# Kernel optimization log

Hardware: AMD Instinct MI355X
Metric: run time of the kernel (lower is better)

Reference implementation:

```python
import jax, jax.numpy as jnp
import numpy as np

H = 1024        # hidden_size
I = 512         # moe_intermediate_size
E = 16          # n_routed_experts
K = 2           # num_experts_per_tok
N_SHARED = 2    # n_shared_experts
IS = I * N_SHARED  # shared expert intermediate
B, S = 2, 2048


def setup_inputs() -> dict:
    key = jax.random.key(0)
    ks = jax.random.split(key, 9)
    sc = 0.02
    return {
        "hidden_states": jax.random.normal(ks[0], (B, S, H), jnp.float32),
        "router_w":     jax.random.normal(ks[1], (E, H), jnp.float32) * sc,
        "expert_gate":  jax.random.normal(ks[2], (E, H, I), jnp.float32) * sc,
        "expert_up":    jax.random.normal(ks[3], (E, H, I), jnp.float32) * sc,
        "expert_down":  jax.random.normal(ks[4], (E, I, H), jnp.float32) * sc,
        "shared_gate":  jax.random.normal(ks[5], (H, IS), jnp.float32) * sc,
        "shared_up":    jax.random.normal(ks[6], (H, IS), jnp.float32) * sc,
        "shared_down":  jax.random.normal(ks[7], (IS, H), jnp.float32) * sc,
    }


def reference(hidden_states, router_w, expert_gate, expert_up, expert_down,
              shared_gate, shared_up, shared_down):
    orig_shape = hidden_states.shape
    x = hidden_states.reshape(-1, H)            # [T, H]
    T = x.shape[0]

    # --- MoEGate: softmax router scores, top-k, normalized weights ---
    scores = jax.nn.softmax(x @ router_w.T, axis=-1)        # [T, E]
    topk_w, topk_idx = jax.lax.top_k(scores, K)             # [T, K]
    topk_w = topk_w / jnp.sum(topk_w, axis=-1, keepdims=True)  # norm_topk_prob

    # Sparse combine weights as dense [T, E] gate matrix (scatter of top-k).
    gates = jnp.zeros((T, E), x.dtype).at[jnp.arange(T)[:, None], topk_idx].add(topk_w)

    # --- Routed experts: gated SiLU MLP per expert, weighted combine ---
    g = jnp.einsum('th,ehi->tei', x, expert_gate)           # [T, E, I]
    u = jnp.einsum('th,ehi->tei', x, expert_up)             # [T, E, I]
    a = jax.nn.silu(g) * u                                  # [T, E, I]
    y = jnp.einsum('tei,eih,te->th', a, expert_down, gates) # [T, H]

    # --- Shared experts ---
    s = (jax.nn.silu(x @ shared_gate) * (x @ shared_up)) @ shared_down  # [T, H]

    return (y + s).reshape(orig_shape)
```

## Files before the change

kernel.cpp:

```cpp
#include <hip/hip_runtime.h>
#include <math.h>

#define H_DIM 1024
#define I_DIM 512
#define E_NUM 16
#define T_TOK 4096
#define IS_DIM 1024
#define CSTR 32

#define P_RT   1024
#define P_WU   (P_RT + 2048)
#define P_SG   (P_WU + 2048)
#define P_SU   (P_SG + 256)
#define P_END  (P_SU + 256)

#define G_GEMM 1152
#define G_TR   2304
#define G_END  (G_GEMM + G_TR)

#define D_GRID 896

typedef unsigned short u16;
typedef __attribute__((ext_vector_type(8))) short short8;
typedef __attribute__((ext_vector_type(4))) float floatx4;

__device__ __forceinline__ float bf2f(u16 u) {
    union { unsigned int u; float f; } c; c.u = ((unsigned int)u) << 16; return c.f;
}
__device__ __forceinline__ u16 f2bf(float f) {
    union { float f; unsigned int u; } c; c.f = f;
    unsigned int r = (c.u + 0x7fffu + ((c.u >> 16) & 1u)) >> 16;
    return (u16)r;
}
__device__ __forceinline__ void gld16(const u16* g, u16* l) {
    __builtin_amdgcn_global_load_lds(
        (const __attribute__((address_space(1))) unsigned int*)g,
        (__attribute__((address_space(3))) unsigned int*)l, 16, 0, 0);
}

__device__ __forceinline__ void tr64(const float* src, u16* dst, int R, int C,
                                     int local, u16* tile)
{
    int tpm = (R >> 6) * (C >> 6);
    int mat = local / tpm;
    int tl_ = local - mat * tpm;
    int tcn = C >> 6;
    int tr = tl_ / tcn, tc = tl_ - tr * tcn;
    src += (size_t)mat * R * C;
    dst += (size_t)mat * R * C;
    int t = threadIdx.x;
    int r0 = t >> 2, c0 = (t & 3) << 4;
    const float* sp = src + (size_t)(tr * 64 + r0) * C + tc * 64 + c0;
    #pragma unroll
    for (int j = 0; j < 16; j += 4) {
        float4 v = *(const float4*)(sp + j);
        tile[r0 * 65 + c0 + j + 0] = f2bf(v.x);
        tile[r0 * 65 + c0 + j + 1] = f2bf(v.y);
        tile[r0 * 65 + c0 + j + 2] = f2bf(v.z);
        tile[r0 * 65 + c0 + j + 3] = f2bf(v.w);
    }
    __syncthreads();
    int cW = t >> 2, rW = (t & 3) << 4;
    u16 tmp[16];
    #pragma unroll
    for (int j = 0; j < 16; ++j) tmp[j] = tile[(rW + j) * 65 + cW];
    u16* dp = dst + (size_t)(tc * 64 + cW) * R + tr * 64 + rW;
    *(uint4*)(dp)     = *(const uint4*)(tmp);
    *(uint4*)(dp + 8) = *(const uint4*)(tmp + 8);
}

__device__ __forceinline__ int derive_routed(int gi, const int* cnt,
                                             int& e, int& mt, int& sub, int& abase)
{
    int off = 0, b = 0;
    #pragma unroll
    for (int ee = 0; ee < E_NUM; ++ee) {
        int mts = (cnt[ee * CSTR] + 127) >> 7;
        int span = mts << 3;
        if (gi < off + span) {
            int local = gi - off;
            e = ee; mt = local >> 3; sub = local & 7; abase = b;
            return 1;
        }
        off += span; b += mts << 7;
    }
    return 0;
}

__global__ __launch_bounds__(256, 4)
void k_prep(const float* x, const float* rw,
            const float* wg, const float* wu, const float* sg, const float* su,
            u16* wgt, u16* wut, u16* sgt, u16* sut,
            u16* xb, float* topkw, int* elist, int* cnt)
{
    __shared__ u16 tile[64 * 65];
    int bi = blockIdx.x;
    if (bi >= P_RT) {
        if (bi < P_WU)      tr64(wg, wgt, 1024, 512,  bi - P_RT, tile);
        else if (bi < P_SG) tr64(wu, wut, 1024, 512,  bi - P_WU, tile);
        else if (bi < P_SU) tr64(sg, sgt, 1024, 1024, bi - P_SG, tile);
        else                tr64(su, sut, 1024, 1024, bi - P_SU, tile);
        return;
    }
    int lane = threadIdx.x & 63;
    int wv = threadIdx.x >> 6;
    int t = bi * 4 + wv;
    const float* xr = x + (size_t)t * H_DIM;
    float xv[16];
    #pragma unroll
    for (int j = 0; j < 16; ++j) xv[j] = xr[j * 64 + lane];
    u16* xrow = xb + (size_t)t * H_DIM;
    #pragma unroll
    for (int j = 0; j < 16; ++j) xrow[j * 64 + lane] = f2bf(xv[j]);
    float sc[E_NUM];
    #pragma unroll
    for (int e = 0; e < E_NUM; ++e) sc[e] = 0.f;
    #pragma unroll
    for (int e = 0; e < E_NUM; ++e) {
        const float* rr = rw + e * H_DIM;
        #pragma unroll
        for (int j = 0; j < 16; ++j) sc[e] += xv[j] * rr[j * 64 + lane];
    }
    #pragma unroll
    for (int off = 32; off > 0; off >>= 1) {
        float tmp[E_NUM];
        #pragma unroll
        for (int e = 0; e < E_NUM; ++e) tmp[e] = __shfl_xor(sc[e], off, 64);
        #pragma unroll
        for (int e = 0; e < E_NUM; ++e) sc[e] += tmp[e];
    }
    if (lane == 0) {
        float b1 = -1e30f, b2 = -1e30f; int i1 = 0, i2 = 0;
        #pragma unroll
        for (int e = 0; e < E_NUM; ++e) {
            if (sc[e] > b1) { b2 = b1; i2 = i1; b1 = sc[e]; i1 = e; }
            else if (sc[e] > b2) { b2 = sc[e]; i2 = e; }
        }
        float w1 = 1.f / (1.f + __expf(b2 - b1));
        float w2 = 1.f - w1;
        topkw[t * 2]     = w1;
        topkw[t * 2 + 1] = w2;
        int p1 = atomicAdd(&cnt[i1 * CSTR], 1); elist[i1 * T_TOK + p1] = (t << 1);
        int p2 = atomicAdd(&cnt[i2 * CSTR], 1); elist[i2 * T_TOK + p2] = (t << 1) | 1;
    }
}

__global__ __launch_bounds__(256, 2)
void k_gateup(const u16* xb, const u16* wgt, const u16* wut,
              const u16* sgt, const u16* sut,
              const float* wd, const float* sd, u16* wdt, u16* sdt,
              const int* elist, const int* cnt,
              u16* act, u16* sact)
{
    __shared__ u16 smem[32768];
    int bi = blockIdx.x;
    if (bi >= G_GEMM) {
        int tb = bi - G_GEMM;
        if (tb < 2048) tr64(wd, wdt, 512, 1024, tb, smem);
        else           tr64(sd, sdt, 1024, 1024, tb - 2048, smem);
        return;
    }
    int kind, e = 0, mt, cb, abase = 0;
    if (bi < 512) { kind = 1; mt = bi >> 4; cb = bi & 15; }
    else {
        kind = 0;
        if (!derive_routed(bi - 512, cnt, e, mt, cb, abase)) return;
    }

    int tid = threadIdx.x, lane = tid & 63, w = tid >> 6;
    int srow = lane >> 2, scp = lane & 3;

    const u16* gb = kind ? sgt : (wgt + (size_t)e * I_DIM * H_DIM);
    const u16* ub = kind ? sut : (wut + (size_t)e * I_DIM * H_DIM);
    int c = cnt[e * CSTR];

    const u16 *gA0, *gA1, *gG, *gU;
    int oA0, oA1, oG, oU;
    {
        int row0 = (w * 2) * 16 + srow;
        int row1 = (w * 2 + 1) * 16 + srow;
        int gc0 = scp ^ ((row0 >> 1) & 3);
        int gc1 = scp ^ ((row1 >> 1) & 3);
        int tok0, tok1;
        if (kind) { tok0 = mt * 128 + row0; tok1 = mt * 128 + row1; }
        else {
            int p0 = mt * 128 + row0; int pc0 = p0 < c ? p0 : c - 1;
            int p1 = mt * 128 + row1; int pc1 = p1 < c ? p1 : c - 1;
            tok0 = elist[e * T_TOK + pc0] >> 1;
            tok1 = elist[e * T_TOK + pc1] >> 1;
        }
        gA0 = xb + (size_t)tok0 * H_DIM + gc0 * 8;
        gA1 = xb + (size_t)tok1 * H_DIM + gc1 * 8;
        oA0 = (w * 2) * 512;
        oA1 = (w * 2 + 1) * 512;
        int rw_ = w * 16 + srow;
        int gcw = scp ^ ((rw_ >> 1) & 3);
        gG = gb + (size_t)(cb * 64 + rw_) * H_DIM + gcw * 8;
        gU = ub + (size_t)(cb * 64 + rw_) * H_DIM + gcw * 8;
        oG = 8192 + w * 512;
        oU = 12288 + w * 512;
    }

    int wr = w >> 1, wc = w & 1;
    int quad = lane >> 4, l15 = lane & 15;
    int fA[4], fG[2], fU[2];
    #pragma unroll
    for (int i = 0; i < 4; ++i) {
        int r = wr * 64 + i * 16 + l15;
        fA[i] = r * 32 + (quad ^ ((r >> 1) & 3)) * 8;
    }
    #pragma unroll
    for (int j = 0; j < 2; ++j) {
        int n = wc * 32 + j * 16 + l15;
        fG[j] = 8192  + n * 32 + (quad ^ ((n >> 1) & 3)) * 8;
        fU[j] = 12288 + n * 32 + (quad ^ ((n >> 1) & 3)) * 8;
    }

    floatx4 accg[4][2], accu[4][2];
    #pragma unroll
    for (int i = 0; i < 4; ++i)
        #pragma unroll
        for (int j = 0; j < 2; ++j)
            #pragma unroll
            for (int r = 0; r < 4; ++r) { accg[i][j][r] = 0.f; accu[i][j][r] = 0.f; }

#define STAGE_GU(bsel) { \
    u16* sb = smem + (bsel) * 16384; \
    _Pragma("unroll") \
    for (int q = 0; q < 2; ++q) { \
        gld16(gA0 + q * 32, sb + oA0 + q * 4096); \
        gld16(gA1 + q * 32, sb + oA1 + q * 4096); \
        gld16(gG  + q * 32, sb + oG  + q * 2048); \
        gld16(gU  + q * 32, sb + oU  + q * 2048); \
    } \
    gA0 += 64; gA1 += 64; gG += 64; gU += 64; }

    STAGE_GU(0);
    __syncthreads();
    for (int s = 0; s < H_DIM / 64; ++s) {
        int cur = s & 1;
        if (s + 1 < H_DIM / 64) STAGE_GU(cur ^ 1);
        const u16* cbuf = smem + cur * 16384;
        #pragma unroll
        for (int q = 0; q < 2; ++q) {
            short8 a[4], g[2], u[2];
            #pragma unroll
            for (int i = 0; i < 4; ++i) a[i] = *(const short8*)(cbuf + fA[i] + q * 4096);
            #pragma unroll
            for (int j = 0; j < 2; ++j) {
                g[j] = *(const short8*)(cbuf + fG[j] + q * 2048);
                u[j] = *(const short8*)(cbuf + fU[j] + q * 2048);
            }
            #pragma unroll
            for (int i = 0; i < 4; ++i)
                #pragma unroll
                for (int j = 0; j < 2; ++j) {
                    accg[i][j] = __builtin_amdgcn_mfma_f32_16x16x32_bf16(a[i], g[j], accg[i][j], 0, 0, 0);
                    accu[i][j] = __builtin_amdgcn_mfma_f32_16x16x32_bf16(a[i], u[j], accu[i][j], 0, 0, 0);
                }
        }
        __syncthreads();
    }
#undef STAGE_GU

    u16* obase = kind ? (sact + (size_t)(mt * 128) * IS_DIM)
                      : (act + (size_t)(abase + mt * 128) * I_DIM);
    int old = kind ? IS_DIM : I_DIM;
    #pragma unroll
    for (int i = 0; i < 4; ++i)
        #pragma unroll
        for (int j = 0; j < 2; ++j)
            #pragma unroll
            for (int r = 0; r < 4; ++r) {
                int row = wr * 64 + i * 16 + quad * 4 + r;
                int col = cb * 64 + wc * 32 + j * 16 + l15;
                float gg = accg[i][j][r], uu = accu[i][j][r];
                float aa = gg / (1.f + __expf(-gg)) * uu;
                obase[(size_t)row * old + col] = f2bf(aa);
            }
}

__global__ __launch_bounds__(256, 2)
void k_down(const u16* act, const u16* sact, const u16* wdt, const u16* sdt,
            const int* elist, const int* cnt, const float* topkw,
            u16* y0, u16* y1, float* out)
{
    int bi = blockIdx.x;
    int kind, e = 0, mt, nb, abase = 0;
    if (bi < 256) { kind = 1; mt = bi >> 3; nb = bi & 7; }
    else {
        kind = 0;
        if (!derive_routed(bi - 256, cnt, e, mt, nb, abase)) return;
    }

    __shared__ u16 smem[32768];
    int tid = threadIdx.x, lane = tid & 63, w = tid >> 6;
    int srow = lane >> 2, scp = lane & 3;

    int K = kind ? IS_DIM : I_DIM;
    const u16* ab = kind ? (sact + (size_t)(mt * 128) * IS_DIM)
                         : (act + (size_t)(abase + mt * 128) * I_DIM);
    const u16* bb = kind ? (sdt + (size_t)(nb * 128) * IS_DIM)
                         : (wdt + ((size_t)e * H_DIM + nb * 128) * I_DIM);
    int c = cnt[e * CSTR];

    const u16 *gA0, *gA1, *gB0, *gB1;
    int oA0, oA1, oB0, oB1;
    {
        int row0 = (w * 2) * 16 + srow;
        int row1 = (w * 2 + 1) * 16 + srow;
        int gc0 = scp ^ ((row0 >> 1) & 3);
        int gc1 = scp ^ ((row1 >> 1) & 3);
        gA0 = ab + (size_t)row0 * K + gc0 * 8;
        gA1 = ab + (size_t)row1 * K + gc1 * 8;
        gB0 = bb + (size_t)row0 * K + gc0 * 8;
        gB1 = bb + (size_t)row1 * K + gc1 * 8;
        oA0 = (w * 2) * 512;
        oA1 = (w * 2 + 1) * 512;
        oB0 = 8192 + (w * 2) * 512;
        oB1 = 8192 + (w * 2 + 1) * 512;
    }

    int wr = w >> 1, wc = w & 1;
    int quad = lane >> 4, l15 = lane & 15;
    int fA[4], fB[4];
    #pragma unroll
    for (int i = 0; i < 4; ++i) {
        int r = wr * 64 + i * 16 + l15;
        fA[i] = r * 32 + (quad ^ ((r >> 1) & 3)) * 8;
    }
    #pragma unroll
    for (int j = 0; j < 4; ++j) {
        int n = wc * 64 + j * 16 + l15;
        fB[j] = 8192 + n * 32 + (quad ^ ((n >> 1) & 3)) * 8;
    }

    floatx4 acc[4][4];
    #pragma unroll
    for (int i = 0; i < 4; ++i)
        #pragma unroll
        for (int j = 0; j < 4; ++j)
            #pragma unroll
            for (int r = 0; r < 4; ++r) acc[i][j][r] = 0.f;

#define STAGE_DN(bsel) { \
    u16* sb = smem + (bsel) * 16384; \
    _Pragma("unroll") \
    for (int q = 0; q < 2; ++q) { \
        gld16(gA0 + q * 32, sb + oA0 + q * 4096); \
        gld16(gA1 + q * 32, sb + oA1 + q * 4096); \
        gld16(gB0 + q * 32, sb + oB0 + q * 4096); \
        gld16(gB1 + q * 32, sb + oB1 + q * 4096); \
    } \
    gA0 += 64; gA1 += 64; gB0 += 64; gB1 += 64; }

    int steps = K >> 6;
    STAGE_DN(0);
    __syncthreads();
    for (int s = 0; s < steps; ++s) {
        int cur = s & 1;
        if (s + 1 < steps) STAGE_DN(cur ^ 1);
        const u16* cbuf = smem + cur * 16384;
        #pragma unroll
        for (int q = 0; q < 2; ++q) {
            short8 a[4], b[4];
            #pragma unroll
            for (int i = 0; i < 4; ++i) a[i] = *(const short8*)(cbuf + fA[i] + q * 4096);
            #pragma unroll
            for (int j = 0; j < 4; ++j) b[j] = *(const short8*)(cbuf + fB[j] + q * 4096);
            #pragma unroll
            for (int i = 0; i < 4; ++i)
                #pragma unroll
                for (int j = 0; j < 4; ++j)
                    acc[i][j] = __builtin_amdgcn_mfma_f32_16x16x32_bf16(a[i], b[j], acc[i][j], 0, 0, 0);
        }
        __syncthreads();
    }
#undef STAGE_DN

    if (kind) {
        #pragma unroll
        for (int i = 0; i < 4; ++i)
            #pragma unroll
            for (int j = 0; j < 4; ++j)
                #pragma unroll
                for (int r = 0; r < 4; ++r) {
                    int row = mt * 128 + wr * 64 + i * 16 + quad * 4 + r;
                    int col = nb * 128 + wc * 64 + j * 16 + l15;
                    out[(size_t)row * H_DIM + col] = acc[i][j][r];
                }
    } else {
        #pragma unroll
        for (int i = 0; i < 4; ++i)
            #pragma unroll
            for (int r = 0; r < 4; ++r) {
                int row = wr * 64 + i * 16 + quad * 4 + r;
                int p = mt * 128 + row;
                if (p < c) {
                    int ent = elist[e * T_TOK + p];
                    int t = ent >> 1, sl = ent & 1;
                    float wt = topkw[t * 2 + sl];
                    u16* yb = sl ? y1 : y0;
                    #pragma unroll
                    for (int j = 0; j < 4; ++j) {
                        int col = nb * 128 + wc * 64 + j * 16 + l15;
                        yb[(size_t)t * H_DIM + col] = f2bf(wt * acc[i][j][r]);
                    }
                }
            }
    }
}

__global__ __launch_bounds__(256)
void k_final(float* out, const u16* y0, const u16* y1)
{
    int i = blockIdx.x * 256 + threadIdx.x;
    float4 o = ((const float4*)out)[i];
    uint2 a = ((const uint2*)y0)[i];
    uint2 b = ((const uint2*)y1)[i];
    const u16* pa = (const u16*)&a;
    const u16* pb = (const u16*)&b;
    o.x += bf2f(pa[0]) + bf2f(pb[0]);
    o.y += bf2f(pa[1]) + bf2f(pb[1]);
    o.z += bf2f(pa[2]) + bf2f(pb[2]);
    o.w += bf2f(pa[3]) + bf2f(pb[3]);
    ((float4*)out)[i] = o;
}

extern "C" void kernel_launch(void* const* d_in, const int* in_sizes, int n_in,
                              void* d_out, int out_size, void* d_ws, size_t ws_size,
                              hipStream_t stream)
{
    const float* x  = (const float*)d_in[0];
    const float* rw = (const float*)d_in[1];
    const float* wg = (const float*)d_in[2];
    const float* wu = (const float*)d_in[3];
    const float* wd = (const float*)d_in[4];
    const float* sg = (const float*)d_in[5];
    const float* su = (const float*)d_in[6];
    const float* sd = (const float*)d_in[7];
    float* out = (float*)d_out;

    char* ws = (char*)d_ws;
    const size_t MB = 1024ull * 1024ull;
    u16* wgt  = (u16*)(ws);
    u16* wut  = (u16*)(ws + 16 * MB);
    u16* wdt  = (u16*)(ws + 32 * MB);
    u16* sgt  = (u16*)(ws + 48 * MB);
    u16* sut  = (u16*)(ws + 50 * MB);
    u16* sdt  = (u16*)(ws + 52 * MB);
    u16* xb   = (u16*)(ws + 54 * MB);
    u16* act  = (u16*)(ws + 62 * MB);
    u16* sact = (u16*)(ws + 72 * MB);
    u16* y0   = (u16*)(ws + 80 * MB);
    u16* y1   = (u16*)(ws + 88 * MB);
    float* topkw  = (float*)(ws + 96 * MB);
    int* elist    = (int*)(ws + 96 * MB + 64 * 1024);
    int* cnt      = (int*)(ws + 97 * MB);

    hipMemsetAsync(cnt, 0, E_NUM * CSTR * sizeof(int), stream);
    k_prep<<<P_END, 256, 0, stream>>>(x, rw, wg, wu, sg, su,
                                      wgt, wut, sgt, sut,
                                      xb, topkw, elist, cnt);
    k_gateup<<<G_END, 256, 0, stream>>>(xb, wgt, wut, sgt, sut,
                                        wd, sd, wdt, sdt,
                                        elist, cnt, act, sact);
    k_down<<<D_GRID, 256, 0, stream>>>(act, sact, wdt, sdt,
                                       elist, cnt, topkw, y0, y1, out);
    k_final<<<T_TOK * H_DIM / 4 / 256, 256, 0, stream>>>(out, y0, y1);
}
```

Before: 278.2 us.

## Halve K-step LDS tiles, add explicit waitcnt pipelining, fuse combine via atomics

```diff
diff --git a/kernel.cpp b/kernel.cpp
--- a/kernel.cpp
+++ b/kernel.cpp
@@ -23,6 +23,11 @@
 typedef unsigned short u16;
 typedef __attribute__((ext_vector_type(8))) short short8;
 typedef __attribute__((ext_vector_type(4))) float floatx4;
+
+#define VM4   asm volatile("s_waitcnt vmcnt(4)" ::: "memory")
+#define VM0   asm volatile("s_waitcnt vmcnt(0)" ::: "memory")
+#define LGKM0 asm volatile("s_waitcnt lgkmcnt(0)" ::: "memory")
+#define BAR   __builtin_amdgcn_s_barrier()
 
 __device__ __forceinline__ float bf2f(u16 u) {
     union { unsigned int u; float f; } c; c.u = ((unsigned int)u) << 16; return c.f;
@@ -145,14 +150,14 @@
     }
 }
 
-__global__ __launch_bounds__(256, 2)
+__global__ __launch_bounds__(256, 4)
 void k_gateup(const u16* xb, const u16* wgt, const u16* wut,
               const u16* sgt, const u16* sut,
               const float* wd, const float* sd, u16* wdt, u16* sdt,
               const int* elist, const int* cnt,
               u16* act, u16* sact)
 {
-    __shared__ u16 smem[32768];
+    __shared__ u16 smem[16384];
     int bi = blockIdx.x;
     if (bi >= G_GEMM) {
         int tb = bi - G_GEMM;
@@ -197,8 +202,8 @@
         int gcw = scp ^ ((rw_ >> 1) & 3);
         gG = gb + (size_t)(cb * 64 + rw_) * H_DIM + gcw * 8;
         gU = ub + (size_t)(cb * 64 + rw_) * H_DIM + gcw * 8;
-        oG = 8192 + w * 512;
-        oU = 12288 + w * 512;
+        oG = 4096 + w * 512;
+        oU = 6144 + w * 512;
     }
 
     int wr = w >> 1, wc = w & 1;
@@ -212,8 +217,8 @@
     #pragma unroll
     for (int j = 0; j < 2; ++j) {
         int n = wc * 32 + j * 16 + l15;
-        fG[j] = 8192  + n * 32 + (quad ^ ((n >> 1) & 3)) * 8;
-        fU[j] = 12288 + n * 32 + (quad ^ ((n >> 1) & 3)) * 8;
+        fG[j] = 4096 + n * 32 + (quad ^ ((n >> 1) & 3)) * 8;
+        fU[j] = 6144 + n * 32 + (quad ^ ((n >> 1) & 3)) * 8;
     }
 
     floatx4 accg[4][2], accu[4][2];
@@ -225,41 +230,38 @@
             for (int r = 0; r < 4; ++r) { accg[i][j][r] = 0.f; accu[i][j][r] = 0.f; }
 
 #define STAGE_GU(bsel) { \
-    u16* sb = smem + (bsel) * 16384; \
-    _Pragma("unroll") \
-    for (int q = 0; q < 2; ++q) { \
-        gld16(gA0 + q * 32, sb + oA0 + q * 4096); \
-        gld16(gA1 + q * 32, sb + oA1 + q * 4096); \
-        gld16(gG  + q * 32, sb + oG  + q * 2048); \
-        gld16(gU  + q * 32, sb + oU  + q * 2048); \
-    } \
-    gA0 += 64; gA1 += 64; gG += 64; gU += 64; }
+    u16* sb = smem + (bsel) * 8192; \
+    gld16(gA0, sb + oA0); \
+    gld16(gA1, sb + oA1); \
+    gld16(gG,  sb + oG); \
+    gld16(gU,  sb + oU); \
+    gA0 += 32; gA1 += 32; gG += 32; gU += 32; }
 
     STAGE_GU(0);
-    __syncthreads();
-    for (int s = 0; s < H_DIM / 64; ++s) {
-        int cur = s & 1;
-        if (s + 1 < H_DIM / 64) STAGE_GU(cur ^ 1);
-        const u16* cbuf = smem + cur * 16384;
-        #pragma unroll
-        for (int q = 0; q < 2; ++q) {
-            short8 a[4], g[2], u[2];
-            #pragma unroll
-            for (int i = 0; i < 4; ++i) a[i] = *(const short8*)(cbuf + fA[i] + q * 4096);
+    const int nt = H_DIM / 32;
+    for (int t = 0; t < nt; ++t) {
+        int cur = t & 1;
+        if (t + 1 < nt) { STAGE_GU(cur ^ 1); VM4; }
+        else            { VM0; }
+        BAR;
+        const u16* cbuf = smem + cur * 8192;
+        short8 a[4], g[2], u[2];
+        #pragma unroll
+        for (int i = 0; i < 4; ++i) a[i] = *(const short8*)(cbuf + fA[i]);
+        #pragma unroll
+        for (int j = 0; j < 2; ++j) {
+            g[j] = *(const short8*)(cbuf + fG[j]);
+            u[j] = *(const short8*)(cbuf + fU[j]);
+        }
+        #pragma unroll
+        for (int i = 0; i < 4; ++i)
             #pragma unroll
             for (int j = 0; j < 2; ++j) {
-                g[j] = *(const short8*)(cbuf + fG[j] + q * 2048);
-                u[j] = *(const short8*)(cbuf + fU[j] + q * 2048);
+                accg[i][j] = __builtin_amdgcn_mfma_f32_16x16x32_bf16(a[i], g[j], accg[i][j], 0, 0, 0);
+                accu[i][j] = __builtin_amdgcn_mfma_f32_16x16x32_bf16(a[i], u[j], accu[i][j], 0, 0, 0);
             }
-            #pragma unroll
-            for (int i = 0; i < 4; ++i)
-                #pragma unroll
-                for (int j = 0; j < 2; ++j) {
-                    accg[i][j] = __builtin_amdgcn_mfma_f32_16x16x32_bf16(a[i], g[j], accg[i][j], 0, 0, 0);
-                    accu[i][j] = __builtin_amdgcn_mfma_f32_16x16x32_bf16(a[i], u[j], accu[i][j], 0, 0, 0);
-                }
-        }
-        __syncthreads();
+        LGKM0;
+        BAR;
     }
 #undef STAGE_GU
 
@@ -280,10 +282,10 @@
             }
 }
 
-__global__ __launch_bounds__(256, 2)
+__global__ __launch_bounds__(256, 3)
 void k_down(const u16* act, const u16* sact, const u16* wdt, const u16* sdt,
             const int* elist, const int* cnt, const float* topkw,
-            u16* y0, u16* y1, float* out)
+            float* out)
 {
     int bi = blockIdx.x;
     int kind, e = 0, mt, nb, abase = 0;
@@ -293,7 +295,7 @@
         if (!derive_routed(bi - 256, cnt, e, mt, nb, abase)) return;
     }
 
-    __shared__ u16 smem[32768];
+    __shared__ u16 smem[16384];
     int tid = threadIdx.x, lane = tid & 63, w = tid >> 6;
     int srow = lane >> 2, scp = lane & 3;
 
@@ -317,8 +319,8 @@
         gB1 = bb + (size_t)row1 * K + gc1 * 8;
         oA0 = (w * 2) * 512;
         oA1 = (w * 2 + 1) * 512;
-        oB0 = 8192 + (w * 2) * 512;
-        oB1 = 8192 + (w * 2 + 1) * 512;
+        oB0 = 4096 + (w * 2) * 512;
+        oB1 = 4096 + (w * 2 + 1) * 512;
     }
 
     int wr = w >> 1, wc = w & 1;
@@ -332,7 +334,7 @@
     #pragma unroll
     for (int j = 0; j < 4; ++j) {
         int n = wc * 64 + j * 16 + l15;
-        fB[j] = 8192 + n * 32 + (quad ^ ((n >> 1) & 3)) * 8;
+        fB[j] = 4096 + n * 32 + (quad ^ ((n >> 1) & 3)) * 8;
     }
 
     floatx4 acc[4][4];
@@ -344,37 +346,33 @@
             for (int r = 0; r < 4; ++r) acc[i][j][r] = 0.f;
 
 #define STAGE_DN(bsel) { \
-    u16* sb = smem + (bsel) * 16384; \
-    _Pragma("unroll") \
-    for (int q = 0; q < 2; ++q) { \
-        gld16(gA0 + q * 32, sb + oA0 + q * 4096); \
-        gld16(gA1 + q * 32, sb + oA1 + q * 4096); \
-        gld16(gB0 + q * 32, sb + oB0 + q * 4096); \
-        gld16(gB1 + q * 32, sb + oB1 + q * 4096); \
-    } \
-    gA0 += 64; gA1 += 64; gB0 += 64; gB1 += 64; }
-
-    int steps = K >> 6;
+    u16* sb = smem + (bsel) * 8192; \
+    gld16(gA0, sb + oA0); \
+    gld16(gA1, sb + oA1); \
+    gld16(gB0, sb + oB0); \
+    gld16(gB1, sb + oB1); \
+    gA0 += 32; gA1 += 32; gB0 += 32; gB1 += 32; }
+
+    int nt = K >> 5;
     STAGE_DN(0);
-    __syncthreads();
-    for (int s = 0; s < steps; ++s) {
-        int cur = s & 1;
-        if (s + 1 < steps) STAGE_DN(cur ^ 1);
-        const u16* cbuf = smem + cur * 16384;
-        #pragma unroll
-        for (int q = 0; q < 2; ++q) {
-            short8 a[4], b[4];
-            #pragma unroll
-            for (int i = 0; i < 4; ++i) a[i] = *(const short8*)(cbuf + fA[i] + q * 4096);
-            #pragma unroll
-            for (int j = 0; j < 4; ++j) b[j] = *(const short8*)(cbuf + fB[j] + q * 4096);
-            #pragma unroll
-            for (int i = 0; i < 4; ++i)
-                #pragma unroll
-                for (int j = 0; j < 4; ++j)
-                    acc[i][j] = __builtin_amdgcn_mfma_f32_16x16x32_bf16(a[i], b[j], acc[i][j], 0, 0, 0);
-        }
-        __syncthreads();
+    for (int t = 0; t < nt; ++t) {
+        int cur = t & 1;
+        if (t + 1 < nt) { STAGE_DN(cur ^ 1); VM4; }
+        else            { VM0; }
+        BAR;
+        const u16* cbuf = smem + cur * 8192;
+        short8 a[4], b[4];
+        #pragma unroll
+        for (int i = 0; i < 4; ++i) a[i] = *(const short8*)(cbuf + fA[i]);
+        #pragma unroll
+        for (int j = 0; j < 4; ++j) b[j] = *(const short8*)(cbuf + fB[j]);
+        #pragma unroll
+        for (int i = 0; i < 4; ++i)
+            #pragma unroll
+            for (int j = 0; j < 4; ++j)
+                acc[i][j] = __builtin_amdgcn_mfma_f32_16x16x32_bf16(a[i], b[j], acc[i][j], 0, 0, 0);
+        LGKM0;
+        BAR;
     }
 #undef STAGE_DN
 
@@ -387,7 +385,7 @@
                 for (int r = 0; r < 4; ++r) {
                     int row = mt * 128 + wr * 64 + i * 16 + quad * 4 + r;
                     int col = nb * 128 + wc * 64 + j * 16 + l15;
-                    out[(size_t)row * H_DIM + col] = acc[i][j][r];
+                    atomicAdd(&out[(size_t)row * H_DIM + col], acc[i][j][r]);
                 }
     } else {
         #pragma unroll
@@ -400,31 +398,14 @@
                     int ent = elist[e * T_TOK + p];
                     int t = ent >> 1, sl = ent & 1;
                     float wt = topkw[t * 2 + sl];
-                    u16* yb = sl ? y1 : y0;
                     #pragma unroll
                     for (int j = 0; j < 4; ++j) {
                         int col = nb * 128 + wc * 64 + j * 16 + l15;
-                        yb[(size_t)t * H_DIM + col] = f2bf(wt * acc[i][j][r]);
+                        atomicAdd(&out[(size_t)t * H_DIM + col], wt * acc[i][j][r]);
                     }
                 }
             }
     }
-}
-
-__global__ __launch_bounds__(256)
-void k_final(float* out, const u16* y0, const u16* y1)
-{
-    int i = blockIdx.x * 256 + threadIdx.x;
-    float4 o = ((const float4*)out)[i];
-    uint2 a = ((const uint2*)y0)[i];
-    uint2 b = ((const uint2*)y1)[i];
-    const u16* pa = (const u16*)&a;
-    const u16* pb = (const u16*)&b;
-    o.x += bf2f(pa[0]) + bf2f(pb[0]);
-    o.y += bf2f(pa[1]) + bf2f(pb[1]);
-    o.z += bf2f(pa[2]) + bf2f(pb[2]);
-    o.w += bf2f(pa[3]) + bf2f(pb[3]);
-    ((float4*)out)[i] = o;
 }
 
 extern "C" void kernel_launch(void* const* d_in, const int* in_sizes, int n_in,
@@ -452,13 +433,12 @@
     u16* xb   = (u16*)(ws + 54 * MB);
     u16* act  = (u16*)(ws + 62 * MB);
     u16* sact = (u16*)(ws + 72 * MB);
-    u16* y0   = (u16*)(ws + 80 * MB);
-    u16* y1   = (u16*)(ws + 88 * MB);
     float* topkw  = (float*)(ws + 96 * MB);
     int* elist    = (int*)(ws + 96 * MB + 64 * 1024);
     int* cnt      = (int*)(ws + 97 * MB);
 
     hipMemsetAsync(cnt, 0, E_NUM * CSTR * sizeof(int), stream);
+    hipMemsetAsync(out, 0, (size_t)T_TOK * H_DIM * sizeof(float), stream);
     k_prep<<<P_END, 256, 0, stream>>>(x, rw, wg, wu, sg, su,
                                       wgt, wut, sgt, sut,
                                       xb, topkw, elist, cnt);
@@ -466,6 +446,5 @@
                                         wd, sd, wdt, sdt,
                                         elist, cnt, act, sact);
     k_down<<<D_GRID, 256, 0, stream>>>(act, sact, wdt, sdt,
-                                       elist, cnt, topkw, y0, y1, out);
-    k_final<<<T_TOK * H_DIM / 4 / 256, 256, 0, stream>>>(out, y0, y1);
-}
+                                       elist, cnt, topkw, out);
+}
```

Measured after the change: 296.2 us. 1.06x slower.

## Load weight operands directly into registers, shrink LDS, raise occupancy

Applied to the files above, without the earlier changes.

```diff
diff --git a/kernel.cpp b/kernel.cpp
--- a/kernel.cpp
+++ b/kernel.cpp
@@ -23,6 +23,11 @@
 typedef unsigned short u16;
 typedef __attribute__((ext_vector_type(8))) short short8;
 typedef __attribute__((ext_vector_type(4))) float floatx4;
+
+#define VM6   asm volatile("s_waitcnt vmcnt(6)" ::: "memory")
+#define VM0   asm volatile("s_waitcnt vmcnt(0)" ::: "memory")
+#define LGKM0 asm volatile("s_waitcnt lgkmcnt(0)" ::: "memory")
+#define BAR   __builtin_amdgcn_s_barrier()
 
 __device__ __forceinline__ float bf2f(u16 u) {
     union { unsigned int u; float f; } c; c.u = ((unsigned int)u) << 16; return c.f;
@@ -145,14 +150,14 @@
     }
 }
 
-__global__ __launch_bounds__(256, 2)
+__global__ __launch_bounds__(256, 3)
 void k_gateup(const u16* xb, const u16* wgt, const u16* wut,
               const u16* sgt, const u16* sut,
               const float* wd, const float* sd, u16* wdt, u16* sdt,
               const int* elist, const int* cnt,
               u16* act, u16* sact)
 {
-    __shared__ u16 smem[32768];
+    __shared__ u16 smem[8192];
     int bi = blockIdx.x;
     if (bi >= G_GEMM) {
         int tb = bi - G_GEMM;
@@ -174,8 +179,8 @@
     const u16* ub = kind ? sut : (wut + (size_t)e * I_DIM * H_DIM);
     int c = cnt[e * CSTR];
 
-    const u16 *gA0, *gA1, *gG, *gU;
-    int oA0, oA1, oG, oU;
+    const u16 *gA0, *gA1;
+    int oA0, oA1;
     {
         int row0 = (w * 2) * 16 + srow;
         int row1 = (w * 2 + 1) * 16 + srow;
@@ -193,28 +198,20 @@
         gA1 = xb + (size_t)tok1 * H_DIM + gc1 * 8;
         oA0 = (w * 2) * 512;
         oA1 = (w * 2 + 1) * 512;
-        int rw_ = w * 16 + srow;
-        int gcw = scp ^ ((rw_ >> 1) & 3);
-        gG = gb + (size_t)(cb * 64 + rw_) * H_DIM + gcw * 8;
-        gU = ub + (size_t)(cb * 64 + rw_) * H_DIM + gcw * 8;
-        oG = 8192 + w * 512;
-        oU = 12288 + w * 512;
     }
 
     int wr = w >> 1, wc = w & 1;
     int quad = lane >> 4, l15 = lane & 15;
-    int fA[4], fG[2], fU[2];
+    int fA[4];
     #pragma unroll
     for (int i = 0; i < 4; ++i) {
         int r = wr * 64 + i * 16 + l15;
         fA[i] = r * 32 + (quad ^ ((r >> 1) & 3)) * 8;
     }
-    #pragma unroll
-    for (int j = 0; j < 2; ++j) {
-        int n = wc * 32 + j * 16 + l15;
-        fG[j] = 8192  + n * 32 + (quad ^ ((n >> 1) & 3)) * 8;
-        fU[j] = 12288 + n * 32 + (quad ^ ((n >> 1) & 3)) * 8;
-    }
+    const u16* bG0 = gb + (size_t)(cb * 64 + wc * 32 + 0  + l15) * H_DIM + quad * 8;
+    const u16* bG1 = gb + (size_t)(cb * 64 + wc * 32 + 16 + l15) * H_DIM + quad * 8;
+    const u16* bU0 = ub + (size_t)(cb * 64 + wc * 32 + 0  + l15) * H_DIM + quad * 8;
+    const u16* bU1 = ub + (size_t)(cb * 64 + wc * 32 + 16 + l15) * H_DIM + quad * 8;
 
     floatx4 accg[4][2], accu[4][2];
     #pragma unroll
@@ -224,44 +221,52 @@
             #pragma unroll
             for (int r = 0; r < 4; ++r) { accg[i][j][r] = 0.f; accu[i][j][r] = 0.f; }
 
-#define STAGE_GU(bsel) { \
-    u16* sb = smem + (bsel) * 16384; \
+    short8 gS[2][2], uS[2][2];
+
+#define STAGEA(bsel, kk) { \
+    u16* sb = smem + (bsel) * 4096; \
+    gld16(gA0 + (kk), sb + oA0); \
+    gld16(gA1 + (kk), sb + oA1); }
+
+#define LOADB(set, kk) { \
+    gS[set][0] = *(const short8*)(bG0 + (kk)); \
+    gS[set][1] = *(const short8*)(bG1 + (kk)); \
+    uS[set][0] = *(const short8*)(bU0 + (kk)); \
+    uS[set][1] = *(const short8*)(bU1 + (kk)); }
+
+#define COMPUTE_GU(bsel, set) { \
+    const u16* cb_ = smem + (bsel) * 4096; \
+    short8 a_[4]; \
     _Pragma("unroll") \
-    for (int q = 0; q < 2; ++q) { \
-        gld16(gA0 + q * 32, sb + oA0 + q * 4096); \
-        gld16(gA1 + q * 32, sb + oA1 + q * 4096); \
-        gld16(gG  + q * 32, sb + oG  + q * 2048); \
-        gld16(gU  + q * 32, sb + oU  + q * 2048); \
-    } \
-    gA0 += 64; gA1 += 64; gG += 64; gU += 64; }
-
-    STAGE_GU(0);
-    __syncthreads();
-    for (int s = 0; s < H_DIM / 64; ++s) {
-        int cur = s & 1;
-        if (s + 1 < H_DIM / 64) STAGE_GU(cur ^ 1);
-        const u16* cbuf = smem + cur * 16384;
-        #pragma unroll
-        for (int q = 0; q < 2; ++q) {
-            short8 a[4], g[2], u[2];
-            #pragma unroll
-            for (int i = 0; i < 4; ++i) a[i] = *(const short8*)(cbuf + fA[i] + q * 4096);
-            #pragma unroll
-            for (int j = 0; j < 2; ++j) {
-                g[j] = *(const short8*)(cbuf + fG[j] + q * 2048);
-                u[j] = *(const short8*)(cbuf + fU[j] + q * 2048);
-            }
-            #pragma unroll
-            for (int i = 0; i < 4; ++i)
-                #pragma unroll
-                for (int j = 0; j < 2; ++j) {
-                    accg[i][j] = __builtin_amdgcn_mfma_f32_16x16x32_bf16(a[i], g[j], accg[i][j], 0, 0, 0);
-                    accu[i][j] = __builtin_amdgcn_mfma_f32_16x16x32_bf16(a[i], u[j], accu[i][j], 0, 0, 0);
-                }
-        }
-        __syncthreads();
-    }
-#undef STAGE_GU
+    for (int i_ = 0; i_ < 4; ++i_) a_[i_] = *(const short8*)(cb_ + fA[i_]); \
+    _Pragma("unroll") \
+    for (int i_ = 0; i_ < 4; ++i_) { \
+        accg[i_][0] = __builtin_amdgcn_mfma_f32_16x16x32_bf16(a_[i_], gS[set][0], accg[i_][0], 0, 0, 0); \
+        accg[i_][1] = __builtin_amdgcn_mfma_f32_16x16x32_bf16(a_[i_], gS[set][1], accg[i_][1], 0, 0, 0); \
+        accu[i_][0] = __builtin_amdgcn_mfma_f32_16x16x32_bf16(a_[i_], uS[set][0], accu[i_][0], 0, 0, 0); \
+        accu[i_][1] = __builtin_amdgcn_mfma_f32_16x16x32_bf16(a_[i_], uS[set][1], accu[i_][1], 0, 0, 0); \
+    } }
+
+    STAGEA(0, 0);
+    LOADB(0, 0);
+    const int nt = H_DIM / 32;
+    for (int t = 0; t < nt; t += 2) {
+        { int k1 = (t + 1) * 32;
+          STAGEA(1, k1); LOADB(1, k1); VM6; }
+        BAR;
+        COMPUTE_GU(0, 0);
+        LGKM0; BAR;
+        if (t + 2 < nt) {
+            int k2 = (t + 2) * 32;
+            STAGEA(0, k2); LOADB(0, k2); VM6;
+        } else VM0;
+        BAR;
+        COMPUTE_GU(1, 1);
+        LGKM0; BAR;
+    }
+#undef STAGEA
+#undef LOADB
+#undef COMPUTE_GU
 
     u16* obase = kind ? (sact + (size_t)(mt * 128) * IS_DIM)
                       : (act + (size_t)(abase + mt * 128) * I_DIM);
@@ -280,7 +285,7 @@
             }
 }
 
-__global__ __launch_bounds__(256, 2)
+__global__ __launch_bounds__(256, 3)
 void k_down(const u16* act, const u16* sact, const u16* wdt, const u16* sdt,
             const int* elist, const int* cnt, const float* topkw,
             u16* y0, u16* y1, float* out)
@@ -293,7 +298,7 @@
         if (!derive_routed(bi - 256, cnt, e, mt, nb, abase)) return;
     }
 
-    __shared__ u16 smem[32768];
+    __shared__ u16 smem[8192];
     int tid = threadIdx.x, lane = tid & 63, w = tid >> 6;
     int srow = lane >> 2, scp = lane & 3;
 
@@ -304,8 +309,8 @@
                          : (wdt + ((size_t)e * H_DIM + nb * 128) * I_DIM);
     int c = cnt[e * CSTR];
 
-    const u16 *gA0, *gA1, *gB0, *gB1;
-    int oA0, oA1, oB0, oB1;
+    const u16 *gA0, *gA1;
+    int oA0, oA1;
     {
         int row0 = (w * 2) * 16 + srow;
         int row1 = (w * 2 + 1) * 16 + srow;
@@ -313,27 +318,22 @@
         int gc1 = scp ^ ((row1 >> 1) & 3);
         gA0 = ab + (size_t)row0 * K + gc0 * 8;
         gA1 = ab + (size_t)row1 * K + gc1 * 8;
-        gB0 = bb + (size_t)row0 * K + gc0 * 8;
-        gB1 = bb + (size_t)row1 * K + gc1 * 8;
         oA0 = (w * 2) * 512;
         oA1 = (w * 2 + 1) * 512;
-        oB0 = 8192 + (w * 2) * 512;
-        oB1 = 8192 + (w * 2 + 1) * 512;
     }
 
     int wr = w >> 1, wc = w & 1;
     int quad = lane >> 4, l15 = lane & 15;
-    int fA[4], fB[4];
+    int fA[4];
     #pragma unroll
     for (int i = 0; i < 4; ++i) {
         int r = wr * 64 + i * 16 + l15;
         fA[i] = r * 32 + (quad ^ ((r >> 1) & 3)) * 8;
     }
-    #pragma unroll
-    for (int j = 0; j < 4; ++j) {
-        int n = wc * 64 + j * 16 + l15;
-        fB[j] = 8192 + n * 32 + (quad ^ ((n >> 1) & 3)) * 8;
-    }
+    const u16* bB0 = bb + (size_t)(nb * 0 + wc * 64 + 0  + l15) * K + quad * 8;
+    const u16* bB1 = bb + (size_t)(wc * 64 + 16 + l15) * K + quad * 8;
+    const u16* bB2 = bb + (size_t)(wc * 64 + 32 + l15) * K + quad * 8;
+    const u16* bB3 = bb + (size_t)(wc * 64 + 48 + l15) * K + quad * 8;
 
     floatx4 acc[4][4];
     #pragma unroll
@@ -343,40 +343,52 @@
             #pragma unroll
             for (int r = 0; r < 4; ++r) acc[i][j][r] = 0.f;
 
-#define STAGE_DN(bsel) { \
-    u16* sb = smem + (bsel) * 16384; \
+    short8 bS[2][4];
+
+#define STAGEA(bsel, kk) { \
+    u16* sb = smem + (bsel) * 4096; \
+    gld16(gA0 + (kk), sb + oA0); \
+    gld16(gA1 + (kk), sb + oA1); }
+
+#define LOADB(set, kk) { \
+    bS[set][0] = *(const short8*)(bB0 + (kk)); \
+    bS[set][1] = *(const short8*)(bB1 + (kk)); \
+    bS[set][2] = *(const short8*)(bB2 + (kk)); \
+    bS[set][3] = *(const short8*)(bB3 + (kk)); }
+
+#define COMPUTE_DN(bsel, set) { \
+    const u16* cb_ = smem + (bsel) * 4096; \
+    short8 a_[4]; \
     _Pragma("unroll") \
-    for (int q = 0; q < 2; ++q) { \
-        gld16(gA0 + q * 32, sb + oA0 + q * 4096); \
-        gld16(gA1 + q * 32, sb + oA1 + q * 4096); \
-        gld16(gB0 + q * 32, sb + oB0 + q * 4096); \
-        gld16(gB1 + q * 32, sb + oB1 + q * 4096); \
-    } \
-    gA0 += 64; gA1 += 64; gB0 += 64; gB1 += 64; }
-
-    int steps = K >> 6;
-    STAGE_DN(0);
-    __syncthreads();
-    for (int s = 0; s < steps; ++s) {
-        int cur = s & 1;
-        if (s + 1 < steps) STAGE_DN(cur ^ 1);
-        const u16* cbuf = smem + cur * 16384;
-        #pragma unroll
-        for (int q = 0; q < 2; ++q) {
-            short8 a[4], b[4];
-            #pragma unroll
-            for (int i = 0; i < 4; ++i) a[i] = *(const short8*)(cbuf + fA[i] + q * 4096);
-            #pragma unroll
-            for (int j = 0; j < 4; ++j) b[j] = *(const short8*)(cbuf + fB[j] + q * 4096);
-            #pragma unroll
-            for (int i = 0; i < 4; ++i)
-                #pragma unroll
-                for (int j = 0; j < 4; ++j)
-                    acc[i][j] = __builtin_amdgcn_mfma_f32_16x16x32_bf16(a[i], b[j], acc[i][j], 0, 0, 0);
-        }
-        __syncthreads();
-    }
-#undef STAGE_DN
+    for (int i_ = 0; i_ < 4; ++i_) a_[i_] = *(const short8*)(cb_ + fA[i_]); \
+    _Pragma("unroll") \
+    for (int i_ = 0; i_ < 4; ++i_) { \
+        acc[i_][0] = __builtin_amdgcn_mfma_f32_16x16x32_bf16(a_[i_], bS[set][0], acc[i_][0], 0, 0, 0); \
+        acc[i_][1] = __builtin_amdgcn_mfma_f32_16x16x32_bf16(a_[i_], bS[set][1], acc[i_][1], 0, 0, 0); \
+        acc[i_][2] = __builtin_amdgcn_mfma_f32_16x16x32_bf16(a_[i_], bS[set][2], acc[i_][2], 0, 0, 0); \
+        acc[i_][3] = __builtin_amdgcn_mfma_f32_16x16x32_bf16(a_[i_], bS[set][3], acc[i_][3], 0, 0, 0); \
+    } }
+
+    const int nt = K >> 5;
+    STAGEA(0, 0);
+    LOADB(0, 0);
+    for (int t = 0; t < nt; t += 2) {
+        { int k1 = (t + 1) * 32;
+          STAGEA(1, k1); LOADB(1, k1); VM6; }
+        BAR;
+        COMPUTE_DN(0, 0);
+        LGKM0; BAR;
+        if (t + 2 < nt) {
+            int k2 = (t + 2) * 32;
+            STAGEA(0, k2); LOADB(0, k2); VM6;
+        } else VM0;
+        BAR;
+        COMPUTE_DN(1, 1);
+        LGKM0; BAR;
+    }
+#undef STAGEA
+#undef LOADB
+#undef COMPUTE_DN
 
     if (kind) {
         #pragma unroll
```

New measurement: 329.3 us. 1.18x slower.
